# Kernel tuning notes

Hardware: AMD Instinct MI355X
Metric: run time of the kernel (lower is better)

## Reference

```python
import jax, jax.numpy as jnp
import numpy as np
from jax import lax

B, IN_N, MID_N, OUT_N, K, L, WH = 16, 256, 256, 256, 3, 4096, 1024
EPS = 1e-5


def att_conv(x, W, b=None):
    # x: [B, Cin, L], W: [B, Cout, Cin, K] -> per-sample conv1d, padding='same'
    pl, pr = (K - 1) // 2, K // 2
    xp = jnp.pad(x, ((0, 0), (0, 0), (pl, pr)))
    out = 0.
    for t in range(K):  # small fixed K, unrolled shifted-slice einsum
        out = out + jnp.einsum('bcl,boc->bol', lax.dynamic_slice_in_dim(xp, t, L, 2), W[..., t])
    if b is not None:
        out = out + b[:, :, None]
    return out


def batch_norm(x, w, b):
    # training-mode BN over (N, L) per channel, biased variance
    mean = x.mean((0, 2), keepdims=True)
    var = ((x - mean) ** 2).mean((0, 2), keepdims=True)
    return (x - mean) * (w[None, :, None] / jnp.sqrt(var + EPS)) + b[None, :, None]


def se_module(x, w1, b1, w2, b2):
    s = x.mean(2, keepdims=True)  # [B, C, 1]
    s = jax.nn.relu(jnp.einsum('bcl,oc->bol', s, w1) + b1[None, :, None])
    s = jax.nn.sigmoid(jnp.einsum('bcl,oc->bol', s, w2) + b2[None, :, None])
    return x * s


def setup_inputs() -> dict:
    key = jax.random.key(0)
    ks = jax.random.split(key, 16)
    f = lambda k, sh, sc=0.02: jax.random.normal(k, sh, jnp.float32) * sc
    return {
        'x': f(ks[0], (B, IN_N, L), 1.0),
        'att1': f(ks[1], (B, MID_N, WH), 1.0),
        'att2': f(ks[2], (B, MID_N, WH), 1.0),
        'att3': f(ks[3], (B, OUT_N, WH), 1.0),
        'w1_w': f(ks[4], (IN_N * K, WH)), 'w1_b': jnp.zeros((IN_N * K,), jnp.float32),
        'w2_w': f(ks[5], (MID_N * K, WH)), 'w2_b': jnp.zeros((MID_N * K,), jnp.float32),
        'w3_w': f(ks[6], (MID_N * K, WH)), 'w3_b': jnp.zeros((MID_N * K,), jnp.float32),
        'b1_w': f(ks[7], (1, WH)), 'b1_b': jnp.zeros((1,), jnp.float32),
        'bn2_w': jnp.full((MID_N,), 0.1, jnp.float32), 'bn2_b': jnp.zeros((MID_N,), jnp.float32),
        'bn3_w': jnp.full((OUT_N,), 0.1, jnp.float32), 'bn3_b': jnp.zeros((OUT_N,), jnp.float32),
        'se1_w': f(ks[8], (OUT_N, OUT_N)), 'se1_b': jnp.zeros((OUT_N,), jnp.float32),
        'se2_w': f(ks[9], (OUT_N, OUT_N)), 'se2_b': jnp.zeros((OUT_N,), jnp.float32),
    }


def reference(x, att1, att2, att3, w1_w, w1_b, w2_w, w2_b, w3_w, w3_b,
              b1_w, b1_b, bn2_w, bn2_b, bn3_w, bn3_b, se1_w, se1_b, se2_w, se2_b):
    shortcut = x  # in_n == out_n, no downsample -> Identity
    # hypernetwork weight generation (Linear on last dim)
    W1 = (att1 @ w1_w.T + w1_b).reshape(B, MID_N, IN_N, K)
    W2 = (att2 @ w2_w.T + w2_b).reshape(B, MID_N, MID_N, K)
    W3 = (att3 @ w3_w.T + w3_b).reshape(B, OUT_N, MID_N, K)
    b1 = (att1 @ b1_w.T + b1_b)[..., 0]  # [B, mid_n]
    h = jax.nn.relu(att_conv(x, W1, b1))
    h = jax.nn.relu(batch_norm(att_conv(h, W2), bn2_w, bn2_b))
    h = jax.nn.relu(batch_norm(att_conv(h, W3), bn3_w, bn3_b))
    out = jax.nn.relu(se_module(h, se1_w, se1_b, se2_w, se2_b) + shortcut)
    return out
```

## Files before the change

kernel.cpp:

```cpp
#include <hip/hip_runtime.h>
#include <hip/hip_bf16.h>

using bf16 = __hip_bfloat16;
typedef __attribute__((ext_vector_type(4))) float f32x4;
typedef __attribute__((ext_vector_type(8))) short short8;
typedef __attribute__((ext_vector_type(2))) unsigned int uint2v;
typedef __attribute__((ext_vector_type(4))) unsigned int uint4v;

#define DEVI static __device__ __forceinline__

DEVI unsigned short f2b(float f){
  unsigned int u = __float_as_uint(f);
  unsigned int r = (u + 0x7fffu + ((u >> 16) & 1u)) >> 16;
  return (unsigned short)r;
}
DEVI float b2f(unsigned short u){
  return __uint_as_float(((unsigned int)u) << 16);
}

DEVI void gload16(const void* g, void* l){
  __builtin_amdgcn_global_load_lds(
      (const __attribute__((address_space(1))) unsigned int*)g,
      (__attribute__((address_space(3))) unsigned int*)l, 16, 0, 0);
}

__global__ __launch_bounds__(256) void k_transpose_x(const float* __restrict__ x,
                                                     bf16* __restrict__ xt)
{
  __shared__ float tile[64][65];
  const int b = blockIdx.z, l0 = blockIdx.x*64, c0 = blockIdx.y*64;
  const int tid = threadIdx.x;
  {
    const int r = tid >> 2, q = tid & 3;
    const float* src = x + ((size_t)(b*256 + c0 + r))*4096 + l0 + q*16;
    #pragma unroll
    for (int j = 0; j < 4; ++j){
      const f32x4 v = *reinterpret_cast<const f32x4*>(src + j*4);
      #pragma unroll
      for (int e = 0; e < 4; ++e) tile[r][q*16 + j*4 + e] = v[e];
    }
  }
  __syncthreads();
  {
    const int jr = tid >> 2, cq = tid & 3;
    unsigned int w[8];
    #pragma unroll
    for (int e = 0; e < 8; ++e){
      const float lo = tile[cq*16 + 2*e][jr];
      const float hi = tile[cq*16 + 2*e + 1][jr];
      w[e] = (unsigned int)f2b(lo) | ((unsigned int)f2b(hi) << 16);
    }
    unsigned short* dst = (unsigned short*)xt + ((size_t)b*4098 + l0 + jr + 1)*256 + c0 + cq*16;
    uint4v a0 = {w[0],w[1],w[2],w[3]}, a1 = {w[4],w[5],w[6],w[7]};
    *reinterpret_cast<uint4v*>(dst)     = a0;
    *reinterpret_cast<uint4v*>(dst + 8) = a1;
  }
}

__global__ void k_zero_pads(bf16* __restrict__ xt, bf16* __restrict__ h1t)
{
  const int b = blockIdx.x, tid = threadIdx.x;
  const size_t top = (size_t)b*4098*256 + tid;
  const size_t bot = (size_t)b*4098*256 + (size_t)4097*256 + tid;
  unsigned short* px = (unsigned short*)xt;
  unsigned short* ph = (unsigned short*)h1t;
  px[top] = 0; px[bot] = 0; ph[top] = 0; ph[bot] = 0;
}

__global__ __launch_bounds__(256) void k_cvt3(const float* __restrict__ s0, const float* __restrict__ s1,
                                              const float* __restrict__ s2, bf16* __restrict__ dst, int n1)
{
  const size_t total = (size_t)3 * (size_t)n1 / 4;
  for (size_t i = (size_t)blockIdx.x*256 + threadIdx.x; i < total; i += (size_t)gridDim.x*256){
    const size_t e = i*4;
    const int which = (int)(e / (size_t)n1);
    const size_t off = e - (size_t)which*(size_t)n1;
    const float* s = which==0 ? s0 : which==1 ? s1 : s2;
    const f32x4 v = *reinterpret_cast<const f32x4*>(s + off);
    uint2v p;
    p[0] = (unsigned)f2b(v[0]) | ((unsigned)f2b(v[1])<<16);
    p[1] = (unsigned)f2b(v[2]) | ((unsigned)f2b(v[3])<<16);
    *reinterpret_cast<uint2v*>((unsigned short*)dst + e) = p;
  }
}

__global__ __launch_bounds__(256) void k_gen(const bf16* __restrict__ attb, const bf16* __restrict__ wbp,
                                             const float* __restrict__ bias0, const float* __restrict__ bias1,
                                             const float* __restrict__ bias2, bf16* __restrict__ Wt)
{
  __shared__ bf16 sA[128*32];
  __shared__ bf16 sB[128*32];
  const int iz = blockIdx.z, i = iz/3, t = iz - i*3;
  const int c0 = blockIdx.y*128, bo0 = blockIdx.x*128;
  const bf16* __restrict__ A  = wbp  + (size_t)i*768*1024;
  const bf16* __restrict__ Bt = attb + (size_t)i*4096*1024;
  const float* __restrict__ bias = (i==0) ? bias0 : (i==1) ? bias1 : bias2;
  const int tid = threadIdx.x, lane = tid & 63, wid = tid >> 6;
  const int wr = wid >> 1, wc = wid & 1;
  const int frow = lane & 15;
  const int sel = (frow >> 1) & 3;
  const int kgs = ((lane >> 4) ^ sel) * 8;
  f32x4 acc[4][4] = {};
  for (int k0 = 0; k0 < 1024; k0 += 32){
    __syncthreads();
    #pragma unroll
    for (int j = 0; j < 2; ++j){
      const int q = tid + j*256, r = q >> 2;
      const int cc = (q & 3) ^ ((r >> 1) & 3);
      gload16(A  + ((size_t)((c0 + r)*3 + t))*1024 + k0 + cc*8, sA + (size_t)q*8);
      gload16(Bt + ((size_t)(bo0 + r))*1024       + k0 + cc*8, sB + (size_t)q*8);
    }
    __syncthreads();
    short8 af[4], bf[4];
    #pragma unroll
    for (int f = 0; f < 4; ++f){
      af[f] = *reinterpret_cast<const short8*>(sA + (size_t)(wr*64 + f*16 + frow)*32 + kgs);
      bf[f] = *reinterpret_cast<const short8*>(sB + (size_t)(wc*64 + f*16 + frow)*32 + kgs);
    }
    #pragma unroll
    for (int fm = 0; fm < 4; ++fm)
      #pragma unroll
      for (int fn = 0; fn < 4; ++fn)
        acc[fm][fn] = __builtin_amdgcn_mfma_f32_16x16x32_bf16(af[fm], bf[fn], acc[fm][fn], 0, 0, 0);
  }
  #pragma unroll
  for (int fm = 0; fm < 4; ++fm){
    const int cb = c0 + wr*64 + fm*16 + (lane >> 4)*4;
    float bi[4];
    #pragma unroll
    for (int j = 0; j < 4; ++j) bi[j] = bias[(cb + j)*3 + t];
    #pragma unroll
    for (int fn = 0; fn < 4; ++fn){
      const int bo = bo0 + wc*64 + fn*16 + frow;
      const int bb = bo >> 8, o = bo & 255;
      unsigned short* dst = (unsigned short*)Wt + ((((size_t)(i*16 + bb)*3 + t)*256 + o)*256 + cb);
      uint2v p;
      p[0] = (unsigned)f2b(acc[fm][fn][0] + bi[0]) | ((unsigned)f2b(acc[fm][fn][1] + bi[1]) << 16);
      p[1] = (unsigned)f2b(acc[fm][fn][2] + bi[2]) | ((unsigned)f2b(acc[fm][fn][3] + bi[3]) << 16);
      *reinterpret_cast<uint2v*>(dst) = p;
    }
  }
}

__global__ __launch_bounds__(256) void k_b1(const float* __restrict__ att1, const float* __restrict__ b1w,
                                            const float* __restrict__ b1b, float* __restrict__ out)
{
  const int m = blockIdx.x*4 + (threadIdx.x >> 6);
  const int lane = threadIdx.x & 63;
  const float* a = att1 + (size_t)m*1024;
  float s = 0.f;
  for (int k = lane*4; k < 1024; k += 256){
    const f32x4 v = *reinterpret_cast<const f32x4*>(a + k);
    const f32x4 w = *reinterpret_cast<const f32x4*>(b1w + k);
    s += v[0]*w[0] + v[1]*w[1] + v[2]*w[2] + v[3]*w[3];
  }
  #pragma unroll
  for (int d = 32; d > 0; d >>= 1) s += __shfl_down(s, d);
  if (lane == 0) out[m] = s + b1b[0];
}

__global__ __launch_bounds__(256) void k_conv(const bf16* __restrict__ Xt, const bf16* __restrict__ W,
                                              const float* __restrict__ bias, bf16* __restrict__ out,
                                              int outBatchStride, int outRowOff, int applyRelu,
                                              float* __restrict__ statSum, float* __restrict__ statSq)
{
  __shared__ bf16 sA[128*32];
  __shared__ bf16 sB[128*32];
  const int b = blockIdx.z, o0 = blockIdx.y*128, l0 = blockIdx.x*128;
  const int tid = threadIdx.x, lane = tid & 63, wid = tid >> 6;
  const int wr = wid >> 1, wc = wid & 1;
  const int frow = lane & 15;
  const int sel = (frow >> 1) & 3;
  const int kgs = ((lane >> 4) ^ sel) * 8;
  f32x4 acc[4][4] = {};
  for (int s = 0; s < 24; ++s){
    const int t = s >> 3, c0 = (s & 7)*32;
    __syncthreads();
    #pragma unroll
    for (int j = 0; j < 2; ++j){
      const int q = tid + j*256, r = q >> 2;
      const int cc = (q & 3) ^ ((r >> 1) & 3);
      gload16(W  + (((size_t)b*3 + t)*256 + o0 + r)*256 + c0 + cc*8, sA + (size_t)q*8);
      gload16(Xt + ((size_t)b*4098 + l0 + t + r)*256    + c0 + cc*8, sB + (size_t)q*8);
    }
    __syncthreads();
    short8 af[4], bf[4];
    #pragma unroll
    for (int f = 0; f < 4; ++f){
      af[f] = *reinterpret_cast<const short8*>(sA + (size_t)(wr*64 + f*16 + frow)*32 + kgs);
      bf[f] = *reinterpret_cast<const short8*>(sB + (size_t)(wc*64 + f*16 + frow)*32 + kgs);
    }
    #pragma unroll
    for (int fm = 0; fm < 4; ++fm)
      #pragma unroll
      for (int fn = 0; fn < 4; ++fn)
        acc[fm][fn] = __builtin_amdgcn_mfma_f32_16x16x32_bf16(af[fm], bf[fn], acc[fm][fn], 0, 0, 0);
  }
  float cs[4][4] = {{0.f}}, cq[4][4] = {{0.f}};
  #pragma unroll
  for (int fm = 0; fm < 4; ++fm){
    const int ob = o0 + wr*64 + fm*16 + (lane >> 4)*4;
    float bi[4] = {0.f, 0.f, 0.f, 0.f};
    if (bias){
      const f32x4 bv = *reinterpret_cast<const f32x4*>(bias + b*256 + ob);
      bi[0]=bv[0]; bi[1]=bv[1]; bi[2]=bv[2]; bi[3]=bv[3];
    }
    #pragma unroll
    for (int fn = 0; fn < 4; ++fn){
      const int l = l0 + wc*64 + fn*16 + frow;
      float v[4];
      #pragma unroll
      for (int j = 0; j < 4; ++j){
        v[j] = acc[fm][fn][j] + bi[j];
        if (applyRelu) v[j] = fmaxf(v[j], 0.f);
        cs[fm][j] += v[j];
        cq[fm][j] += v[j]*v[j];
      }
      unsigned short* dst = (unsigned short*)out +
          ((size_t)b*outBatchStride + (size_t)(l + outRowOff)*256 + ob);
      uint2v p;
      p[0] = (unsigned)f2b(v[0]) | ((unsigned)f2b(v[1]) << 16);
      p[1] = (unsigned)f2b(v[2]) | ((unsigned)f2b(v[3]) << 16);
      *reinterpret_cast<uint2v*>(dst) = p;
    }
  }
  if (statSum){
    #pragma unroll
    for (int fm = 0; fm < 4; ++fm)
      #pragma unroll
      for (int j = 0; j < 4; ++j){
        #pragma unroll
        for (int d = 1; d < 16; d <<= 1){
          cs[fm][j] += __shfl_xor(cs[fm][j], d);
          cq[fm][j] += __shfl_xor(cq[fm][j], d);
        }
      }
    __syncthreads();
    float* ls = (float*)sA;
    float* lq = (float*)sB;
    if (frow == 0){
      const int grp = lane >> 4;
      #pragma unroll
      for (int fm = 0; fm < 4; ++fm)
        #pragma unroll
        for (int j = 0; j < 4; ++j){
          ls[wid*64 + fm*16 + grp*4 + j] = cs[fm][j];
          lq[wid*64 + fm*16 + grp*4 + j] = cq[fm][j];
        }
    }
    __syncthreads();
    if (tid < 128){
      const int wrg = tid >> 6, c6 = tid & 63;
      const float s  = ls[(wrg*2)*64 + c6] + ls[(wrg*2+1)*64 + c6];
      const float qq = lq[(wrg*2)*64 + c6] + lq[(wrg*2+1)*64 + c6];
      atomicAdd(statSum + o0 + tid, s);
      atomicAdd(statSq  + o0 + tid, qq);
    }
  }
}

__global__ void k_bnfin(const float* __restrict__ sum, const float* __restrict__ sq,
                        const float* __restrict__ g, const float* __restrict__ bb,
                        float* __restrict__ scale, float* __restrict__ shift)
{
  const int o = threadIdx.x;
  const float inv = 1.f/65536.f;
  const float m = sum[o]*inv;
  const float v = fmaxf(sq[o]*inv - m*m, 0.f);
  const float sc = g[o] / sqrtf(v + 1e-5f);
  scale[o] = sc;
  shift[o] = bb[o] - m*sc;
}

__global__ __launch_bounds__(256) void k_norm2(const bf16* __restrict__ y, const float* __restrict__ scale,
                                               const float* __restrict__ shift, bf16* __restrict__ h)
{
  const int gr = blockIdx.x*8 + (threadIdx.x >> 5);
  const int oc = threadIdx.x & 31;
  const int b = gr / 4098, lp = gr - b*4098;
  unsigned short* dst = (unsigned short*)h + (size_t)gr*256 + oc*8;
  if (lp == 0 || lp == 4097){
    uint4v z = {0u,0u,0u,0u};
    *reinterpret_cast<uint4v*>(dst) = z;
    return;
  }
  const unsigned short* src = (const unsigned short*)y + ((size_t)b*4096 + (lp-1))*256 + oc*8;
  const uint4v in = *reinterpret_cast<const uint4v*>(src);
  const f32x4 sA0 = *reinterpret_cast<const f32x4*>(scale + oc*8);
  const f32x4 sA1 = *reinterpret_cast<const f32x4*>(scale + oc*8 + 4);
  const f32x4 hA0 = *reinterpret_cast<const f32x4*>(shift + oc*8);
  const f32x4 hA1 = *reinterpret_cast<const f32x4*>(shift + oc*8 + 4);
  uint4v ov;
  #pragma unroll
  for (int e = 0; e < 4; ++e){
    const unsigned int w = in[e];
    const float sc0 = (e<2) ? sA0[2*e] : sA1[2*e-4];
    const float sc1 = (e<2) ? sA0[2*e+1] : sA1[2*e-3];
    const float sh0 = (e<2) ? hA0[2*e] : hA1[2*e-4];
    const float sh1 = (e<2) ? hA0[2*e+1] : hA1[2*e-3];
    const float v0 = fmaxf(b2f((unsigned short)(w & 0xffffu))*sc0 + sh0, 0.f);
    const float v1 = fmaxf(b2f((unsigned short)(w >> 16))*sc1 + sh1, 0.f);
    ov[e] = (unsigned)f2b(v0) | ((unsigned)f2b(v1) << 16);
  }
  *reinterpret_cast<uint4v*>(dst) = ov;
}

__global__ __launch_bounds__(256) void k_norm3(bf16* __restrict__ y, const float* __restrict__ scale,
                                               const float* __restrict__ shift, float* __restrict__ s_sum)
{
  __shared__ float red[8][256];
  const int tid = threadIdx.x;
  const int rr = tid >> 5, oc = tid & 31;
  const size_t row = (size_t)blockIdx.x*8 + rr;
  const int b = (int)(row >> 12);
  unsigned short* p = (unsigned short*)y + row*256 + oc*8;
  const uint4v in = *reinterpret_cast<const uint4v*>(p);
  const f32x4 sA0 = *reinterpret_cast<const f32x4*>(scale + oc*8);
  const f32x4 sA1 = *reinterpret_cast<const f32x4*>(scale + oc*8 + 4);
  const f32x4 hA0 = *reinterpret_cast<const f32x4*>(shift + oc*8);
  const f32x4 hA1 = *reinterpret_cast<const f32x4*>(shift + oc*8 + 4);
  uint4v ov;
  float loc[8];
  #pragma unroll
  for (int e = 0; e < 4; ++e){
    const unsigned int w = in[e];
    const float sc0 = (e<2) ? sA0[2*e] : sA1[2*e-4];
    const float sc1 = (e<2) ? sA0[2*e+1] : sA1[2*e-3];
    const float sh0 = (e<2) ? hA0[2*e] : hA1[2*e-4];
    const float sh1 = (e<2) ? hA0[2*e+1] : hA1[2*e-3];
    const float v0 = fmaxf(b2f((unsigned short)(w & 0xffffu))*sc0 + sh0, 0.f);
    const float v1 = fmaxf(b2f((unsigned short)(w >> 16))*sc1 + sh1, 0.f);
    loc[2*e] = v0; loc[2*e+1] = v1;
    ov[e] = (unsigned)f2b(v0) | ((unsigned)f2b(v1) << 16);
  }
  *reinterpret_cast<uint4v*>(p) = ov;
  #pragma unroll
  for (int j = 0; j < 8; ++j) red[rr][oc*8 + j] = loc[j];
  __syncthreads();
  const int o = tid;
  float tot = 0.f;
  #pragma unroll
  for (int r2 = 0; r2 < 8; ++r2) tot += red[r2][o];
  atomicAdd(&s_sum[(size_t)b*256 + o], tot);
}

__global__ __launch_bounds__(256) void k_se(const float* __restrict__ s_sum, const float* __restrict__ w1,
                                            const float* __restrict__ b1, const float* __restrict__ w2,
                                            const float* __restrict__ b2, float* __restrict__ s2)
{
  __shared__ float sv[256];
  __shared__ float t1[256];
  const int b = blockIdx.x, o = threadIdx.x;
  sv[o] = s_sum[(size_t)b*256 + o] * (1.f/4096.f);
  __syncthreads();
  float a = b1[o];
  for (int c = 0; c < 256; ++c) a += w1[(size_t)o*256 + c] * sv[c];
  t1[o] = fmaxf(a, 0.f);
  __syncthreads();
  float a2 = b2[o];
  for (int c = 0; c < 256; ++c) a2 += w2[(size_t)o*256 + c] * t1[c];
  s2[(size_t)b*256 + o] = 1.f / (1.f + expf(-a2));
}

__global__ __launch_bounds__(256) void k_final(const bf16* __restrict__ h3, const float* __restrict__ s2,
                                               const float* __restrict__ x, float* __restrict__ out)
{
  __shared__ float tile[64][65];
  const int b = blockIdx.z, o0 = blockIdx.y*64, l0 = blockIdx.x*64;
  const int tid = threadIdx.x;
  {
    const int r = tid >> 2, q = tid & 3;
    const unsigned short* src = (const unsigned short*)h3 + ((size_t)b*4096 + l0 + r)*256 + o0 + q*16;
    const uint4v a0 = *reinterpret_cast<const uint4v*>(src);
    const uint4v a1 = *reinterpret_cast<const uint4v*>(src + 8);
    #pragma unroll
    for (int e = 0; e < 4; ++e){
      tile[r][q*16 + 2*e]         = b2f((unsigned short)(a0[e] & 0xffffu));
      tile[r][q*16 + 2*e + 1]     = b2f((unsigned short)(a0[e] >> 16));
      tile[r][q*16 + 8 + 2*e]     = b2f((unsigned short)(a1[e] & 0xffffu));
      tile[r][q*16 + 8 + 2*e + 1] = b2f((unsigned short)(a1[e] >> 16));
    }
  }
  __syncthreads();
  {
    const int orow = tid >> 2, q = tid & 3;
    const int o = o0 + orow;
    const float sc = s2[(size_t)b*256 + o];
    const float* xs = x + ((size_t)b*256 + o)*4096 + l0 + q*16;
    float* dst = out + ((size_t)b*256 + o)*4096 + l0 + q*16;
    #pragma unroll
    for (int k = 0; k < 16; k += 4){
      const f32x4 xv = *reinterpret_cast<const f32x4*>(xs + k);
      f32x4 r;
      #pragma unroll
      for (int e = 0; e < 4; ++e)
        r[e] = fmaxf(tile[q*16 + k + e][orow]*sc + xv[e], 0.f);
      *reinterpret_cast<f32x4*>(dst + k) = r;
    }
  }
}

extern "C" void kernel_launch(void* const* d_in, const int* in_sizes, int n_in,
                              void* d_out, int out_size, void* d_ws, size_t ws_size,
                              hipStream_t stream)
{
  const float* x     = (const float*)d_in[0];
  const float* att1  = (const float*)d_in[1];
  const float* att2  = (const float*)d_in[2];
  const float* att3  = (const float*)d_in[3];
  const float* w1_w  = (const float*)d_in[4];
  const float* w1_b  = (const float*)d_in[5];
  const float* w2_w  = (const float*)d_in[6];
  const float* w2_b  = (const float*)d_in[7];
  const float* w3_w  = (const float*)d_in[8];
  const float* w3_b  = (const float*)d_in[9];
  const float* b1_w  = (const float*)d_in[10];
  const float* b1_b  = (const float*)d_in[11];
  const float* bn2_w = (const float*)d_in[12];
  const float* bn2_b = (const float*)d_in[13];
  const float* bn3_w = (const float*)d_in[14];
  const float* bn3_b = (const float*)d_in[15];
  const float* se1_w = (const float*)d_in[16];
  const float* se1_b = (const float*)d_in[17];
  const float* se2_w = (const float*)d_in[18];
  const float* se2_b = (const float*)d_in[19];

  char* ws = (char*)d_ws;
  bf16*  xT   = (bf16*)(ws + 0);
  bf16*  h1T  = (bf16*)(ws + 33570816);
  bf16*  y2T  = (bf16*)(ws + 67141632);
  bf16*  h2T  = (bf16*)(ws + 100696064);
  bf16*  Wt   = (bf16*)(ws + 134266880);
  bf16*  attb = (bf16*)(ws + 153141248);
  bf16*  wb   = (bf16*)(ws + 178307072);
  float* b1v  = (float*)(ws + 183025664);
  float* st   = (float*)(ws + 183042048);
  float* bn2sum = st;
  float* bn2sq  = st + 256;
  float* bn3sum = st + 512;
  float* bn3sq  = st + 768;
  float* s_sum  = st + 1024;
  float* scale2 = st + 5120;
  float* shift2 = st + 5376;
  float* scale3 = st + 5632;
  float* shift3 = st + 5888;
  float* s2v    = st + 6144;
  bf16*  y3T  = (bf16*)(ws + 0);

  hipMemsetAsync(st, 0, 5120*sizeof(float), stream);

  k_transpose_x<<<dim3(64,4,16),256,0,stream>>>(x, xT);
  k_zero_pads<<<16,256,0,stream>>>(xT, h1T);
  k_cvt3<<<2048,256,0,stream>>>(att1, att2, att3, attb, 4096*1024);
  k_cvt3<<<512,256,0,stream>>>(w1_w, w2_w, w3_w, wb, 768*1024);
  k_gen<<<dim3(32,2,9),256,0,stream>>>(attb, wb, w1_b, w2_b, w3_b, Wt);
  k_b1<<<1024,256,0,stream>>>(att1, b1_w, b1_b, b1v);

  k_conv<<<dim3(32,2,16),256,0,stream>>>(xT,  Wt,                           b1v,     h1T, 4098*256, 1, 1, nullptr, nullptr);
  k_conv<<<dim3(32,2,16),256,0,stream>>>(h1T, Wt + (size_t)1*16*3*256*256,  nullptr, y2T, 4096*256, 0, 0, bn2sum, bn2sq);
  k_bnfin<<<1,256,0,stream>>>(bn2sum, bn2sq, bn2_w, bn2_b, scale2, shift2);
  k_norm2<<<8196,256,0,stream>>>(y2T, scale2, shift2, h2T);
  k_conv<<<dim3(32,2,16),256,0,stream>>>(h2T, Wt + (size_t)2*16*3*256*256,  nullptr, y3T, 4096*256, 0, 0, bn3sum, bn3sq);
  k_bnfin<<<1,256,0,stream>>>(bn3sum, bn3sq, bn3_w, bn3_b, scale3, shift3);
  k_norm3<<<8192,256,0,stream>>>(y3T, scale3, shift3, s_sum);
  k_se<<<16,256,0,stream>>>(s_sum, se1_w, se1_b, se2_w, se2_b, s2v);
  k_final<<<dim3(64,4,16),256,0,stream>>>((const bf16*)y3T, s2v, x, (float*)d_out);
}
```

Measured before the change: 350.8 us.

## Retile conv and hypernet GEMMs to 256x256 double-buffered async LDS pipeline

Both the hypernetwork weight-generation GEMM and the per-sample conv GEMM move from 128x128 tiles with a K-step of 32 and 256 threads to 256x256 tiles with a K-step of 64 and 512 threads. Global-to-LDS loads go into two ping-pong buffers, and the next stage is prefetched while explicit vmcnt waits and raw barriers guard the current one. MFMA sections also raise wave priority. The aim is more operand reuse per LDS byte, fewer barriers, and overlap of loads with matrix math. The cost is far fewer blocks (256 for conv, 144 for gen) and about 128KB of LDS per block, so only one block fits per CU. This can leave CUs idle or hurt latency hiding.

Measured after the change: 339.7 us. 1.03x faster.

```diff
diff --git a/kernel.cpp b/kernel.cpp
--- a/kernel.cpp
+++ b/kernel.cpp
@@ -84,59 +84,94 @@
   }
 }
 
-__global__ __launch_bounds__(256) void k_gen(const bf16* __restrict__ attb, const bf16* __restrict__ wbp,
-                                             const float* __restrict__ bias0, const float* __restrict__ bias1,
-                                             const float* __restrict__ bias2, bf16* __restrict__ Wt)
-{
-  __shared__ bf16 sA[128*32];
-  __shared__ bf16 sB[128*32];
+
+__global__ __launch_bounds__(512, 2) void k_gen(const bf16* __restrict__ attb, const bf16* __restrict__ wbp,
+                                                const float* __restrict__ bias0, const float* __restrict__ bias1,
+                                                const float* __restrict__ bias2, bf16* __restrict__ Wt)
+{
+  __shared__ bf16 sA[2][256*64];
+  __shared__ bf16 sB[2][256*64];
   const int iz = blockIdx.z, i = iz/3, t = iz - i*3;
-  const int c0 = blockIdx.y*128, bo0 = blockIdx.x*128;
-  const bf16* __restrict__ A  = wbp  + (size_t)i*768*1024;
-  const bf16* __restrict__ Bt = attb + (size_t)i*4096*1024;
+  const int bo0 = blockIdx.x*256;
+  const bf16* __restrict__ A  = wbp  + (size_t)i*768*1024 + (size_t)t*1024;
+  const bf16* __restrict__ Bt = attb + (size_t)i*4096*1024 + (size_t)bo0*1024;
   const float* __restrict__ bias = (i==0) ? bias0 : (i==1) ? bias1 : bias2;
   const int tid = threadIdx.x, lane = tid & 63, wid = tid >> 6;
-  const int wr = wid >> 1, wc = wid & 1;
-  const int frow = lane & 15;
-  const int sel = (frow >> 1) & 3;
-  const int kgs = ((lane >> 4) ^ sel) * 8;
-  f32x4 acc[4][4] = {};
-  for (int k0 = 0; k0 < 1024; k0 += 32){
-    __syncthreads();
-    #pragma unroll
-    for (int j = 0; j < 2; ++j){
-      const int q = tid + j*256, r = q >> 2;
-      const int cc = (q & 3) ^ ((r >> 1) & 3);
-      gload16(A  + ((size_t)((c0 + r)*3 + t))*1024 + k0 + cc*8, sA + (size_t)q*8);
-      gload16(Bt + ((size_t)(bo0 + r))*1024       + k0 + cc*8, sB + (size_t)q*8);
-    }
-    __syncthreads();
-    short8 af[4], bf[4];
-    #pragma unroll
-    for (int f = 0; f < 4; ++f){
-      af[f] = *reinterpret_cast<const short8*>(sA + (size_t)(wr*64 + f*16 + frow)*32 + kgs);
-      bf[f] = *reinterpret_cast<const short8*>(sB + (size_t)(wc*64 + f*16 + frow)*32 + kgs);
-    }
-    #pragma unroll
-    for (int fm = 0; fm < 4; ++fm)
-      #pragma unroll
-      for (int fn = 0; fn < 4; ++fn)
-        acc[fm][fn] = __builtin_amdgcn_mfma_f32_16x16x32_bf16(af[fm], bf[fn], acc[fm][fn], 0, 0, 0);
-  }
-  #pragma unroll
-  for (int fm = 0; fm < 4; ++fm){
-    const int cb = c0 + wr*64 + fm*16 + (lane >> 4)*4;
+  const int wr = wid >> 2, wc = wid & 3;
+  const int frow = lane & 15, g = lane >> 4;
+  f32x4 acc[8][4] = {};
+
+#define GEN_STAGE(kt, bufi) { \
+    const int kc = (kt)*64; \
+    _Pragma("unroll") \
+    for (int j = 0; j < 4; ++j){ \
+      const int slot = tid + j*512, r = slot >> 3, s7 = slot & 7; \
+      const int cc = (s7 ^ (r & 7)) * 8; \
+      gload16(A + (size_t)r*3072 + kc + cc, &sA[bufi][slot*8]); \
+    } \
+    _Pragma("unroll") \
+    for (int j = 0; j < 4; ++j){ \
+      const int slot = tid + j*512, r = slot >> 3, s7 = slot & 7; \
+      const int cc = (s7 ^ (r & 7)) * 8; \
+      gload16(Bt + (size_t)r*1024 + kc + cc, &sB[bufi][slot*8]); \
+    } \
+  }
+
+  GEN_STAGE(0, 0);
+  #pragma unroll 1
+  for (int kt = 0; kt < 16; ++kt){
+    const int buf = kt & 1;
+    if (kt + 1 < 16){
+      GEN_STAGE(kt+1, buf^1);
+      asm volatile("s_waitcnt vmcnt(8)" ::: "memory");
+    } else {
+      asm volatile("s_waitcnt vmcnt(0)" ::: "memory");
+    }
+    __builtin_amdgcn_s_barrier();
+    __builtin_amdgcn_sched_barrier(0);
+    const bf16* pA = sA[buf];
+    const bf16* pB = sB[buf];
+    #pragma unroll
+    for (int ks = 0; ks < 2; ++ks){
+      short8 bfr[4];
+      #pragma unroll
+      for (int n = 0; n < 4; ++n){
+        const int row = wc*64 + n*16 + frow;
+        const int sl = (ks*4 + g) ^ (row & 7);
+        bfr[n] = *reinterpret_cast<const short8*>(pB + row*64 + sl*8);
+      }
+      __builtin_amdgcn_s_setprio(1);
+      #pragma unroll
+      for (int m = 0; m < 8; ++m){
+        const int row = wr*128 + m*16 + frow;
+        const int sl = (ks*4 + g) ^ (row & 7);
+        const short8 af = *reinterpret_cast<const short8*>(pA + row*64 + sl*8);
+        #pragma unroll
+        for (int n = 0; n < 4; ++n)
+          acc[m][n] = __builtin_amdgcn_mfma_f32_16x16x32_bf16(af, bfr[n], acc[m][n], 0, 0, 0);
+      }
+      __builtin_amdgcn_s_setprio(0);
+    }
+    __builtin_amdgcn_sched_barrier(0);
+    __builtin_amdgcn_s_barrier();
+    __builtin_amdgcn_sched_barrier(0);
+  }
+#undef GEN_STAGE
+
+  #pragma unroll
+  for (int m = 0; m < 8; ++m){
+    const int cb = wr*128 + m*16 + g*4;
     float bi[4];
     #pragma unroll
     for (int j = 0; j < 4; ++j) bi[j] = bias[(cb + j)*3 + t];
     #pragma unroll
-    for (int fn = 0; fn < 4; ++fn){
-      const int bo = bo0 + wc*64 + fn*16 + frow;
+    for (int n = 0; n < 4; ++n){
+      const int bo = bo0 + wc*64 + n*16 + frow;
       const int bb = bo >> 8, o = bo & 255;
       unsigned short* dst = (unsigned short*)Wt + ((((size_t)(i*16 + bb)*3 + t)*256 + o)*256 + cb);
       uint2v p;
-      p[0] = (unsigned)f2b(acc[fm][fn][0] + bi[0]) | ((unsigned)f2b(acc[fm][fn][1] + bi[1]) << 16);
-      p[1] = (unsigned)f2b(acc[fm][fn][2] + bi[2]) | ((unsigned)f2b(acc[fm][fn][3] + bi[3]) << 16);
+      p[0] = (unsigned)f2b(acc[m][n][0] + bi[0]) | ((unsigned)f2b(acc[m][n][1] + bi[1]) << 16);
+      p[1] = (unsigned)f2b(acc[m][n][2] + bi[2]) | ((unsigned)f2b(acc[m][n][3] + bi[3]) << 16);
       *reinterpret_cast<uint2v*>(dst) = p;
     }
   }
@@ -159,62 +194,97 @@
   if (lane == 0) out[m] = s + b1b[0];
 }
 
-__global__ __launch_bounds__(256) void k_conv(const bf16* __restrict__ Xt, const bf16* __restrict__ W,
-                                              const float* __restrict__ bias, bf16* __restrict__ out,
-                                              int outBatchStride, int outRowOff, int applyRelu,
-                                              float* __restrict__ statSum, float* __restrict__ statSq)
-{
-  __shared__ bf16 sA[128*32];
-  __shared__ bf16 sB[128*32];
-  const int b = blockIdx.z, o0 = blockIdx.y*128, l0 = blockIdx.x*128;
+__global__ __launch_bounds__(512, 2) void k_conv(const bf16* __restrict__ Xt, const bf16* __restrict__ W,
+                                                 const float* __restrict__ bias, bf16* __restrict__ out,
+                                                 int outBatchStride, int outRowOff, int applyRelu,
+                                                 float* __restrict__ statSum, float* __restrict__ statSq)
+{
+  __shared__ bf16 sA[2][256*64];
+  __shared__ bf16 sB[2][256*64];
+  const int b = blockIdx.z, l0 = blockIdx.x*256;
   const int tid = threadIdx.x, lane = tid & 63, wid = tid >> 6;
-  const int wr = wid >> 1, wc = wid & 1;
-  const int frow = lane & 15;
-  const int sel = (frow >> 1) & 3;
-  const int kgs = ((lane >> 4) ^ sel) * 8;
-  f32x4 acc[4][4] = {};
-  for (int s = 0; s < 24; ++s){
-    const int t = s >> 3, c0 = (s & 7)*32;
-    __syncthreads();
-    #pragma unroll
-    for (int j = 0; j < 2; ++j){
-      const int q = tid + j*256, r = q >> 2;
-      const int cc = (q & 3) ^ ((r >> 1) & 3);
-      gload16(W  + (((size_t)b*3 + t)*256 + o0 + r)*256 + c0 + cc*8, sA + (size_t)q*8);
-      gload16(Xt + ((size_t)b*4098 + l0 + t + r)*256    + c0 + cc*8, sB + (size_t)q*8);
-    }
-    __syncthreads();
-    short8 af[4], bf[4];
-    #pragma unroll
-    for (int f = 0; f < 4; ++f){
-      af[f] = *reinterpret_cast<const short8*>(sA + (size_t)(wr*64 + f*16 + frow)*32 + kgs);
-      bf[f] = *reinterpret_cast<const short8*>(sB + (size_t)(wc*64 + f*16 + frow)*32 + kgs);
-    }
-    #pragma unroll
-    for (int fm = 0; fm < 4; ++fm)
-      #pragma unroll
-      for (int fn = 0; fn < 4; ++fn)
-        acc[fm][fn] = __builtin_amdgcn_mfma_f32_16x16x32_bf16(af[fm], bf[fn], acc[fm][fn], 0, 0, 0);
-  }
-  float cs[4][4] = {{0.f}}, cq[4][4] = {{0.f}};
-  #pragma unroll
-  for (int fm = 0; fm < 4; ++fm){
-    const int ob = o0 + wr*64 + fm*16 + (lane >> 4)*4;
+  const int wr = wid >> 2, wc = wid & 3;
+  const int frow = lane & 15, g = lane >> 4;
+  f32x4 acc[8][4] = {};
+
+#define CONV_STAGE(kt, bufi) { \
+    const int tt = (kt) >> 2, c0 = ((kt) & 3)*64; \
+    const bf16* Ab = W  + (((size_t)b*3 + tt)*256)*256 + c0; \
+    const bf16* Bb = Xt + ((size_t)b*4098 + l0 + tt)*256 + c0; \
+    _Pragma("unroll") \
+    for (int j = 0; j < 4; ++j){ \
+      const int slot = tid + j*512, r = slot >> 3, s7 = slot & 7; \
+      const int cc = (s7 ^ (r & 7)) * 8; \
+      gload16(Ab + (size_t)r*256 + cc, &sA[bufi][slot*8]); \
+    } \
+    _Pragma("unroll") \
+    for (int j = 0; j < 4; ++j){ \
+      const int slot = tid + j*512, r = slot >> 3, s7 = slot & 7; \
+      const int cc = (s7 ^ (r & 7)) * 8; \
+      gload16(Bb + (size_t)r*256 + cc, &sB[bufi][slot*8]); \
+    } \
+  }
+
+  CONV_STAGE(0, 0);
+  #pragma unroll 1
+  for (int kt = 0; kt < 12; ++kt){
+    const int buf = kt & 1;
+    if (kt + 1 < 12){
+      CONV_STAGE(kt+1, buf^1);
+      asm volatile("s_waitcnt vmcnt(8)" ::: "memory");
+    } else {
+      asm volatile("s_waitcnt vmcnt(0)" ::: "memory");
+    }
+    __builtin_amdgcn_s_barrier();
+    __builtin_amdgcn_sched_barrier(0);
+    const bf16* pA = sA[buf];
+    const bf16* pB = sB[buf];
+    #pragma unroll
+    for (int ks = 0; ks < 2; ++ks){
+      short8 bfr[4];
+      #pragma unroll
+      for (int n = 0; n < 4; ++n){
+        const int row = wc*64 + n*16 + frow;
+        const int sl = (ks*4 + g) ^ (row & 7);
+        bfr[n] = *reinterpret_cast<const short8*>(pB + row*64 + sl*8);
+      }
+      __builtin_amdgcn_s_setprio(1);
+      #pragma unroll
+      for (int m = 0; m < 8; ++m){
+        const int row = wr*128 + m*16 + frow;
+        const int sl = (ks*4 + g) ^ (row & 7);
+        const short8 af = *reinterpret_cast<const short8*>(pA + row*64 + sl*8);
+        #pragma unroll
+        for (int n = 0; n < 4; ++n)
+          acc[m][n] = __builtin_amdgcn_mfma_f32_16x16x32_bf16(af, bfr[n], acc[m][n], 0, 0, 0);
+      }
+      __builtin_amdgcn_s_setprio(0);
+    }
+    __builtin_amdgcn_sched_barrier(0);
+    __builtin_amdgcn_s_barrier();
+    __builtin_amdgcn_sched_barrier(0);
+  }
+#undef CONV_STAGE
+
+  float cs[8][4] = {{0.f}}, cq[8][4] = {{0.f}};
+  #pragma unroll
+  for (int m = 0; m < 8; ++m){
+    const int ob = wr*128 + m*16 + g*4;
     float bi[4] = {0.f, 0.f, 0.f, 0.f};
     if (bias){
       const f32x4 bv = *reinterpret_cast<const f32x4*>(bias + b*256 + ob);
       bi[0]=bv[0]; bi[1]=bv[1]; bi[2]=bv[2]; bi[3]=bv[3];
     }
     #pragma unroll
-    for (int fn = 0; fn < 4; ++fn){
-      const int l = l0 + wc*64 + fn*16 + frow;
+    for (int n = 0; n < 4; ++n){
+      const int l = l0 + wc*64 + n*16 + frow;
       float v[4];
       #pragma unroll
       for (int j = 0; j < 4; ++j){
-        v[j] = acc[fm][fn][j] + bi[j];
+        v[j] = acc[m][n][j] + bi[j];
         if (applyRelu) v[j] = fmaxf(v[j], 0.f);
-        cs[fm][j] += v[j];
-        cq[fm][j] += v[j]*v[j];
+        cs[m][j] += v[j];
+        cq[m][j] += v[j]*v[j];
       }
       unsigned short* dst = (unsigned short*)out +
           ((size_t)b*outBatchStride + (size_t)(l + outRowOff)*256 + ob);
@@ -226,35 +296,38 @@
   }
   if (statSum){
     #pragma unroll
-    for (int fm = 0; fm < 4; ++fm)
+    for (int m = 0; m < 8; ++m)
       #pragma unroll
       for (int j = 0; j < 4; ++j){
         #pragma unroll
         for (int d = 1; d < 16; d <<= 1){
-          cs[fm][j] += __shfl_xor(cs[fm][j], d);
-          cq[fm][j] += __shfl_xor(cq[fm][j], d);
+          cs[m][j] += __shfl_xor(cs[m][j], d);
+          cq[m][j] += __shfl_xor(cq[m][j], d);
         }
       }
     __syncthreads();
-    float* ls = (float*)sA;
-    float* lq = (float*)sB;
+    float* ls = (float*)&sA[0][0];
+    float* lq = ls + 1024;
     if (frow == 0){
-      const int grp = lane >> 4;
-      #pragma unroll
-      for (int fm = 0; fm < 4; ++fm)
+      #pragma unroll
+      for (int m = 0; m < 8; ++m)
         #pragma unroll
         for (int j = 0; j < 4; ++j){
-          ls[wid*64 + fm*16 + grp*4 + j] = cs[fm][j];
-          lq[wid*64 + fm*16 + grp*4 + j] = cq[fm][j];
+          ls[wid*128 + m*16 + g*4 + j] = cs[m][j];
+          lq[wid*128 + m*16 + g*4 + j] = cq[m][j];
         }
     }
     __syncthreads();
-    if (tid < 128){
-      const int wrg = tid >> 6, c6 = tid & 63;
-      const float s  = ls[(wrg*2)*64 + c6] + ls[(wrg*2+1)*64 + c6];
-      const float qq = lq[(wrg*2)*64 + c6] + lq[(wrg*2+1)*64 + c6];
-      atomicAdd(statSum + o0 + tid, s);
-      atomicAdd(statSq  + o0 + tid, qq);
+    if (tid < 256){
+      const int o = tid, half = o >> 7, idx = o & 127;
+      float s = 0.f, qq = 0.f;
+      #pragma unroll
+      for (int wv = 0; wv < 4; ++wv){
+        s  += ls[(half*4 + wv)*128 + idx];
+        qq += lq[(half*4 + wv)*128 + idx];
+      }
+      atomicAdd(statSum + o, s);
+      atomicAdd(statSq  + o, qq);
     }
   }
 }
@@ -453,14 +526,14 @@
   k_zero_pads<<<16,256,0,stream>>>(xT, h1T);
   k_cvt3<<<2048,256,0,stream>>>(att1, att2, att3, attb, 4096*1024);
   k_cvt3<<<512,256,0,stream>>>(w1_w, w2_w, w3_w, wb, 768*1024);
-  k_gen<<<dim3(32,2,9),256,0,stream>>>(attb, wb, w1_b, w2_b, w3_b, Wt);
+  k_gen<<<dim3(16,1,9),512,0,stream>>>(attb, wb, w1_b, w2_b, w3_b, Wt);
   k_b1<<<1024,256,0,stream>>>(att1, b1_w, b1_b, b1v);
 
-  k_conv<<<dim3(32,2,16),256,0,stream>>>(xT,  Wt,                           b1v,     h1T, 4098*256, 1, 1, nullptr, nullptr);
-  k_conv<<<dim3(32,2,16),256,0,stream>>>(h1T, Wt + (size_t)1*16*3*256*256,  nullptr, y2T, 4096*256, 0, 0, bn2sum, bn2sq);
+  k_conv<<<dim3(16,1,16),512,0,stream>>>(xT,  Wt,                           b1v,     h1T, 4098*256, 1, 1, nullptr, nullptr);
+  k_conv<<<dim3(16,1,16),512,0,stream>>>(h1T, Wt + (size_t)1*16*3*256*256,  nullptr, y2T, 4096*256, 0, 0, bn2sum, bn2sq);
   k_bnfin<<<1,256,0,stream>>>(bn2sum, bn2sq, bn2_w, bn2_b, scale2, shift2);
   k_norm2<<<8196,256,0,stream>>>(y2T, scale2, shift2, h2T);
-  k_conv<<<dim3(32,2,16),256,0,stream>>>(h2T, Wt + (size_t)2*16*3*256*256,  nullptr, y3T, 4096*256, 0, 0, bn3sum, bn3sq);
+  k_conv<<<dim3(16,1,16),512,0,stream>>>(h2T, Wt + (size_t)2*16*3*256*256,  nullptr, y3T, 4096*256, 0, 0, bn3sum, bn3sq);
   k_bnfin<<<1,256,0,stream>>>(bn3sum, bn3sq, bn3_w, bn3_b, scale3, shift3);
   k_norm3<<<8192,256,0,stream>>>(y3T, scale3, shift3, s_sum);
   k_se<<<16,256,0,stream>>>(s_sum, se1_w, se1_b, se2_w, se2_b, s2v);
```
